# Performance work log

Hardware: AMD Instinct MI355X
Metric: run time of the kernel (lower is better)

## Reference

```python
import jax, jax.numpy as jnp
import numpy as np

B, S, D = 8, 2048, 512
MINF = 20000.0  # matches tf code's -20000.0 mask constant


def setup_inputs() -> dict:
    key = jax.random.key(0)
    k1, k2, k3 = jax.random.split(key, 3)
    x1 = jax.random.normal(k1, (B, S, D), dtype=jnp.float32)
    x2 = jax.random.normal(k2, (B, S, D), dtype=jnp.float32)
    # glorot_normal init for the learned (S, S) positional kernel
    std = np.sqrt(2.0 / (S + S)).astype(np.float32)
    kernel = jax.random.normal(k3, (S, S), dtype=jnp.float32) * std
    return {"x1": x1, "x2": x2, "kernel": kernel}


def reference(x1, x2, kernel):
    S_ = kernel.shape[0]
    # tf.matmul(kernel, inputs[i]) broadcasts (S,S) @ (B,S,D) -> (B,S,D)
    h1 = jnp.einsum('st,btd->bsd', kernel, x1)
    h2 = jnp.einsum('st,btd->bsd', kernel, x2)
    # att_scores: (B, S, S)
    scores = jnp.einsum('bsd,btd->bst', h1, h2)
    d_k = jnp.asarray(S_, dtype=scores.dtype) ** 0.5
    # upper_m[i,j] = -20000 for j > i (strictly upper), else 0; added BEFORE scaling
    row = jnp.arange(S_)
    mask = jnp.where(row[None, :] > row[:, None], -MINF, 0.0).astype(scores.dtype)
    attn = jax.nn.softmax((scores + mask) / d_k, axis=-1)
    # note: output attends over h1 (not h2), as in the original code
    return jnp.einsum('bst,btd->bsd', attn, h1)
```

## Files before the change

kernel.cpp:

```cpp
#include <hip/hip_runtime.h>
#include <hip/hip_bf16.h>

#define S_DIM 2048
#define D_DIM 512
#define B_DIM 8
#define SCALE 0.02209708691207961f

typedef __hip_bfloat16 bf16;
typedef short bf16x8 __attribute__((ext_vector_type(8)));
typedef float f32x4 __attribute__((ext_vector_type(4)));

__device__ __forceinline__ unsigned short f2b(float f) {
  __hip_bfloat16 h = __float2bfloat16(f);
  return __builtin_bit_cast(unsigned short, h);
}
__device__ __forceinline__ float b2f(unsigned short s) {
  return __bfloat162float(__builtin_bit_cast(__hip_bfloat16, s));
}

__device__ __forceinline__ void load_lds16(const void* g, void* l) {
  __builtin_amdgcn_global_load_lds((const __attribute__((address_space(1))) void*)g,
                                   (__attribute__((address_space(3))) void*)l, 16, 0, 0);
}

__global__ void convert_k(const float* __restrict__ in, bf16* __restrict__ out, int n8) {
  int i = blockIdx.x * blockDim.x + threadIdx.x;
  if (i >= n8) return;
  const float4* p = (const float4*)in;
  float4 a = p[2 * i], b = p[2 * i + 1];
  bf16x8 r;
  r[0] = f2b(a.x); r[1] = f2b(a.y); r[2] = f2b(a.z); r[3] = f2b(a.w);
  r[4] = f2b(b.x); r[5] = f2b(b.y); r[6] = f2b(b.z); r[7] = f2b(b.w);
  ((bf16x8*)out)[i] = r;
}

__global__ void transpose_f2b(const float* __restrict__ in, bf16* __restrict__ out) {
  __shared__ float tile[32][33];
  int b = blockIdx.z;
  int c0 = blockIdx.x * 32;
  int r0 = blockIdx.y * 32;
  const float* ib = in + (size_t)b * S_DIM * D_DIM;
  bf16* ob = out + (size_t)b * S_DIM * D_DIM;
  int lr = threadIdx.x >> 5, lc = threadIdx.x & 31;
#pragma unroll
  for (int i = 0; i < 4; i++)
    tile[lr + i * 8][lc] = ib[(size_t)(r0 + lr + i * 8) * D_DIM + c0 + lc];
  __syncthreads();
#pragma unroll
  for (int i = 0; i < 4; i++) {
    int cc = lr + i * 8;
    ob[(size_t)(c0 + cc) * S_DIM + r0 + lc] = __float2bfloat16(tile[lc][cc]);
  }
}

__global__ void transpose_b2b(const bf16* __restrict__ in, bf16* __restrict__ out) {
  __shared__ bf16 tile[32][33];
  int b = blockIdx.z;
  int c0 = blockIdx.x * 32;
  int r0 = blockIdx.y * 32;
  const bf16* ib = in + (size_t)b * S_DIM * D_DIM;
  bf16* ob = out + (size_t)b * S_DIM * D_DIM;
  int lr = threadIdx.x >> 5, lc = threadIdx.x & 31;
#pragma unroll
  for (int i = 0; i < 4; i++)
    tile[lr + i * 8][lc] = ib[(size_t)(r0 + lr + i * 8) * D_DIM + c0 + lc];
  __syncthreads();
#pragma unroll
  for (int i = 0; i < 4; i++) {
    int cc = lr + i * 8;
    ob[(size_t)(c0 + cc) * S_DIM + r0 + lc] = tile[lc][cc];
  }
}

template <int NT, int LDE>
__device__ __forceinline__ void core256(
    const bf16* __restrict__ Asrc, const bf16* __restrict__ Bsrc,
    char* smem, f32x4 (*acc)[4]) {
  const int tid = threadIdx.x;
  const int w = tid >> 6, L = tid & 63;
  const int l15 = L & 15, lhi = L >> 4;
  const int wr = w >> 2, wn = w & 3;

  const int srow = w * 16 + (L >> 3);
  const int sslot = ((L & 7) ^ ((L >> 3) & 7)) * 8;
  const bf16* pA[2][2];
  const bf16* pB[2][2];
#pragma unroll
  for (int h = 0; h < 2; h++)
#pragma unroll
    for (int ld = 0; ld < 2; ld++) {
      pA[h][ld] = Asrc + (size_t)(h * 128 + srow + ld * 8) * LDE + sslot;
      pB[h][ld] = Bsrc + (size_t)(h * 128 + srow + ld * 8) * LDE + sslot;
    }

  auto stage = [&](int t) {
    char* dA = smem + (t & 1) * 32768 + w * 2048;
    char* dB = smem + 65536 + (t & 1) * 32768 + w * 2048;
    const int ko = t * 64;
#pragma unroll
    for (int h = 0; h < 2; h++)
#pragma unroll
      for (int ld = 0; ld < 2; ld++) {
        load_lds16(pA[h][ld] + ko, dA + h * 16384 + ld * 1024);
        load_lds16(pB[h][ld] + ko, dB + h * 16384 + ld * 1024);
      }
  };

  const int xsw = l15 & 7;
  const int cK0 = (lhi ^ xsw) << 4;
  const int cK1 = ((4 + lhi) ^ xsw) << 4;

  stage(0);
#pragma unroll 2
  for (int t = 0; t < NT; ++t) {
    __syncthreads();
    if (t + 1 < NT) stage(t + 1);
    const char* bA = smem + (t & 1) * 32768;
    const char* bB = smem + 65536 + (t & 1) * 32768;
#pragma unroll
    for (int kk = 0; kk < 2; kk++) {
      const int cK = kk ? cK1 : cK0;
      bf16x8 af[8], bfv[4];
#pragma unroll
      for (int m = 0; m < 8; m++)
        af[m] = *(const bf16x8*)(bA + (wr * 128 + m * 16 + l15) * 128 + cK);
#pragma unroll
      for (int n = 0; n < 4; n++)
        bfv[n] = *(const bf16x8*)(bB + (wn * 64 + n * 16 + l15) * 128 + cK);
      __builtin_amdgcn_s_setprio(1);
#pragma unroll
      for (int m = 0; m < 8; m++)
#pragma unroll
        for (int n = 0; n < 4; n++)
          acc[m][n] = __builtin_amdgcn_mfma_f32_16x16x32_bf16(bfv[n], af[m], acc[m][n], 0, 0, 0);
      __builtin_amdgcn_s_setprio(0);
    }
  }
}

__global__ __launch_bounds__(512, 2) void gemm_h(
    const bf16* __restrict__ A, const bf16* __restrict__ X, bf16* __restrict__ H) {
  extern __shared__ char smem[];
  const int pid = blockIdx.x;
  const int mt = pid & 7;
  const int r_ = pid >> 3;
  const int ntile = r_ & 1;
  const int item = r_ >> 1;
  const int m0 = mt * 256, n0 = ntile * 256;
  const bf16* Asrc = A + (size_t)m0 * S_DIM;
  const bf16* Bsrc = X + (size_t)item * (D_DIM * S_DIM) + (size_t)n0 * S_DIM;
  bf16* Hi = H + (size_t)item * (S_DIM * D_DIM);

  f32x4 acc[8][4];
#pragma unroll
  for (int m = 0; m < 8; m++)
#pragma unroll
    for (int n = 0; n < 4; n++) acc[m][n] = (f32x4){0, 0, 0, 0};

  core256<32, S_DIM>(Asrc, Bsrc, smem, acc);

  const int tid = threadIdx.x;
  const int w = tid >> 6, L = tid & 63;
  const int l15 = L & 15, lhi = L >> 4;
  const int wr = w >> 2, wn = w & 3;
#pragma unroll
  for (int m = 0; m < 8; m++) {
    int grow = m0 + wr * 128 + m * 16 + l15;
#pragma unroll
    for (int n = 0; n < 4; n++) {
      int gcol = n0 + wn * 64 + n * 16 + lhi * 4;
      uint2 u;
      u.x = ((unsigned)f2b(acc[m][n][1]) << 16) | f2b(acc[m][n][0]);
      u.y = ((unsigned)f2b(acc[m][n][3]) << 16) | f2b(acc[m][n][2]);
      *(uint2*)(Hi + (size_t)grow * D_DIM + gcol) = u;
    }
  }
}

__global__ __launch_bounds__(512, 2) void gemm_score(
    const bf16* __restrict__ H1, const bf16* __restrict__ H2,
    bf16* __restrict__ E, float* __restrict__ rowsum) {
  extern __shared__ char smem[];
  const int pid = blockIdx.x;
  const int b = pid & 7;
  const int tri = pid >> 3;
  int mt = (int)((sqrtf(8.0f * (float)tri + 1.0f) - 1.0f) * 0.5f);
  while ((mt + 1) * (mt + 2) / 2 <= tri) mt++;
  while (mt * (mt + 1) / 2 > tri) mt--;
  const int nt = tri - mt * (mt + 1) / 2;
  const int m0 = mt * 256, n0 = nt * 256;
  const bool diag = (mt == nt);
  const bf16* Ab = H1 + (size_t)b * S_DIM * D_DIM;
  const bf16* Bb = H2 + (size_t)b * S_DIM * D_DIM;
  bf16* Eb = E + (size_t)b * S_DIM * S_DIM;
  float* rs = rowsum + b * S_DIM;

  f32x4 acc[8][4];
#pragma unroll
  for (int m = 0; m < 8; m++)
#pragma unroll
    for (int n = 0; n < 4; n++) acc[m][n] = (f32x4){0, 0, 0, 0};

  core256<8, D_DIM>(Ab + (size_t)m0 * D_DIM, Bb + (size_t)n0 * D_DIM, smem, acc);

  const int tid = threadIdx.x;
  const int w = tid >> 6, L = tid & 63;
  const int l15 = L & 15, lhi = L >> 4;
  const int wr = w >> 2, wn = w & 3;
#pragma unroll
  for (int m = 0; m < 8; m++) {
    int sg = m0 + wr * 128 + m * 16 + l15;
    float rp = 0.0f;
#pragma unroll
    for (int n = 0; n < 4; n++) {
      int tg0 = n0 + wn * 64 + n * 16 + lhi * 4;
      unsigned short e[4];
#pragma unroll
      for (int r = 0; r < 4; r++) {
        float v = (!diag || (tg0 + r) <= sg) ? __expf(acc[m][n][r] * SCALE) : 0.0f;
        e[r] = f2b(v);
        rp += b2f(e[r]);
      }
      uint2 u;
      u.x = ((unsigned)e[1] << 16) | e[0];
      u.y = ((unsigned)e[3] << 16) | e[2];
      *(uint2*)(Eb + (size_t)sg * S_DIM + tg0) = u;
    }
    rp += __shfl_xor(rp, 16);
    rp += __shfl_xor(rp, 32);
    if (lhi == 0) atomicAdd(rs + sg, rp);
  }
}

__global__ __launch_bounds__(256, 2) void gemm_pv(
    const bf16* __restrict__ E, const bf16* __restrict__ H1T,
    const float* __restrict__ rowsum, float* __restrict__ out) {
  extern __shared__ char smem[];
  const int pid = blockIdx.x;
  const int b = pid & 7;
  const int r_ = pid >> 3;
  const int nt = r_ & 3;
  const int mb = r_ >> 2;
  const int mt = (mb < 8) ? 2 * mb : 31 - 2 * mb;
  const int m0 = mt * 128, n0 = nt * 128;
  const int NT = (mt + 1) * 2;
  const bf16* Ab = E + (size_t)b * S_DIM * S_DIM + (size_t)m0 * S_DIM;
  const bf16* Bb = H1T + (size_t)b * D_DIM * S_DIM + (size_t)n0 * S_DIM;
  const float* rs = rowsum + b * S_DIM;
  float* Cb = out + (size_t)b * S_DIM * D_DIM;

  const int tid = threadIdx.x;
  const int w = tid >> 6, L = tid & 63;
  const int l15 = L & 15, lhi = L >> 4;
  const int wr = w >> 1, wc = w & 1;

  const int srow = w * 8 + (L >> 3);
  const int sslot = ((L & 7) ^ ((L >> 3) & 7)) * 8;
  const bf16* pA[4];
  const bf16* pB[4];
#pragma unroll
  for (int ld = 0; ld < 4; ld++) {
    pA[ld] = Ab + (size_t)(ld * 32 + srow) * S_DIM + sslot;
    pB[ld] = Bb + (size_t)(ld * 32 + srow) * S_DIM + sslot;
  }

  auto stage = [&](int t) {
    char* dA = smem + (t & 1) * 16384 + w * 1024;
    char* dB = smem + 32768 + (t & 1) * 16384 + w * 1024;
    const int ko = t * 64;
#pragma unroll
    for (int ld = 0; ld < 4; ld++) {
      load_lds16(pA[ld] + ko, dA + ld * 4096);
      load_lds16(pB[ld] + ko, dB + ld * 4096);
    }
  };

  const int xsw = l15 & 7;
  const int cK0 = (lhi ^ xsw) << 4;
  const int cK1 = ((4 + lhi) ^ xsw) << 4;

  f32x4 acc[4][4];
#pragma unroll
  for (int m = 0; m < 4; m++)
#pragma unroll
    for (int n = 0; n < 4; n++) acc[m][n] = (f32x4){0, 0, 0, 0};

  stage(0);
  for (int t = 0; t < NT; ++t) {
    __syncthreads();
    if (t + 1 < NT) stage(t + 1);
    const char* bA = smem + (t & 1) * 16384;
    const char* bB = smem + 32768 + (t & 1) * 16384;
#pragma unroll
    for (int kk = 0; kk < 2; kk++) {
      const int cK = kk ? cK1 : cK0;
      bf16x8 af[4], bfv[4];
#pragma unroll
      for (int m = 0; m < 4; m++)
        af[m] = *(const bf16x8*)(bA + (wr * 64 + m * 16 + l15) * 128 + cK);
#pragma unroll
      for (int n = 0; n < 4; n++)
        bfv[n] = *(const bf16x8*)(bB + (wc * 64 + n * 16 + l15) * 128 + cK);
      __builtin_amdgcn_s_setprio(1);
#pragma unroll
      for (int m = 0; m < 4; m++)
#pragma unroll
        for (int n = 0; n < 4; n++)
          acc[m][n] = __builtin_amdgcn_mfma_f32_16x16x32_bf16(bfv[n], af[m], acc[m][n], 0, 0, 0);
      __builtin_amdgcn_s_setprio(0);
    }
  }

#pragma unroll
  for (int m = 0; m < 4; m++) {
    int sg = m0 + wr * 64 + m * 16 + l15;
    float inv = 1.0f / rs[sg];
#pragma unroll
    for (int n = 0; n < 4; n++) {
      int gcol = n0 + wc * 64 + n * 16 + lhi * 4;
      float4 o;
      o.x = acc[m][n][0] * inv;
      o.y = acc[m][n][1] * inv;
      o.z = acc[m][n][2] * inv;
      o.w = acc[m][n][3] * inv;
      *(float4*)(Cb + (size_t)sg * D_DIM + gcol) = o;
    }
  }
}

extern "C" void kernel_launch(void* const* d_in, const int* in_sizes, int n_in,
                              void* d_out, int out_size, void* d_ws, size_t ws_size,
                              hipStream_t stream) {
  const float* x1 = (const float*)d_in[0];
  const float* x2 = (const float*)d_in[1];
  const float* km = (const float*)d_in[2];
  float* out = (float*)d_out;
  char* ws = (char*)d_ws;
  bf16* E    = (bf16*)(ws);
  bf16* Kbf  = (bf16*)(ws);
  bf16* x1t  = (bf16*)(ws + (8ull << 20));
  bf16* x2t  = (bf16*)(ws + (24ull << 20));
  bf16* h1n  = (bf16*)(ws + (64ull << 20));
  bf16* h2n  = (bf16*)(ws + (80ull << 20));
  bf16* h1t  = (bf16*)(ws + (96ull << 20));
  float* rowsum = (float*)(ws + (112ull << 20));

  convert_k<<<2048, 256, 0, stream>>>(km, Kbf, (S_DIM * S_DIM) / 8);
  transpose_f2b<<<dim3(16, 64, 8), 256, 0, stream>>>(x1, x1t);
  transpose_f2b<<<dim3(16, 64, 8), 256, 0, stream>>>(x2, x2t);
  gemm_h<<<256, 512, 131072, stream>>>(Kbf, x1t, h1n);
  transpose_b2b<<<dim3(16, 64, 8), 256, 0, stream>>>(h1n, h1t);
  hipMemsetAsync(rowsum, 0, B_DIM * S_DIM * sizeof(float), stream);
  gemm_score<<<288, 512, 131072, stream>>>(h1n, h2n, E, rowsum);
  gemm_pv<<<512, 256, 65536, stream>>>(E, h1t, rowsum, out);
}
```

Before: 200.4 us.

## Restructure gemm_h into quadrant-phased pipeline with split staging and explicit waitcnt

```diff
diff --git a/kernel.cpp b/kernel.cpp
--- a/kernel.cpp
+++ b/kernel.cpp
@@ -72,73 +72,7 @@
   }
 }
 
-template <int NT, int LDE>
-__device__ __forceinline__ void core256(
-    const bf16* __restrict__ Asrc, const bf16* __restrict__ Bsrc,
-    char* smem, f32x4 (*acc)[4]) {
-  const int tid = threadIdx.x;
-  const int w = tid >> 6, L = tid & 63;
-  const int l15 = L & 15, lhi = L >> 4;
-  const int wr = w >> 2, wn = w & 3;
-
-  const int srow = w * 16 + (L >> 3);
-  const int sslot = ((L & 7) ^ ((L >> 3) & 7)) * 8;
-  const bf16* pA[2][2];
-  const bf16* pB[2][2];
-#pragma unroll
-  for (int h = 0; h < 2; h++)
-#pragma unroll
-    for (int ld = 0; ld < 2; ld++) {
-      pA[h][ld] = Asrc + (size_t)(h * 128 + srow + ld * 8) * LDE + sslot;
-      pB[h][ld] = Bsrc + (size_t)(h * 128 + srow + ld * 8) * LDE + sslot;
-    }
-
-  auto stage = [&](int t) {
-    char* dA = smem + (t & 1) * 32768 + w * 2048;
-    char* dB = smem + 65536 + (t & 1) * 32768 + w * 2048;
-    const int ko = t * 64;
-#pragma unroll
-    for (int h = 0; h < 2; h++)
-#pragma unroll
-      for (int ld = 0; ld < 2; ld++) {
-        load_lds16(pA[h][ld] + ko, dA + h * 16384 + ld * 1024);
-        load_lds16(pB[h][ld] + ko, dB + h * 16384 + ld * 1024);
-      }
-  };
-
-  const int xsw = l15 & 7;
-  const int cK0 = (lhi ^ xsw) << 4;
-  const int cK1 = ((4 + lhi) ^ xsw) << 4;
-
-  stage(0);
-#pragma unroll 2
-  for (int t = 0; t < NT; ++t) {
-    __syncthreads();
-    if (t + 1 < NT) stage(t + 1);
-    const char* bA = smem + (t & 1) * 32768;
-    const char* bB = smem + 65536 + (t & 1) * 32768;
-#pragma unroll
-    for (int kk = 0; kk < 2; kk++) {
-      const int cK = kk ? cK1 : cK0;
-      bf16x8 af[8], bfv[4];
-#pragma unroll
-      for (int m = 0; m < 8; m++)
-        af[m] = *(const bf16x8*)(bA + (wr * 128 + m * 16 + l15) * 128 + cK);
-#pragma unroll
-      for (int n = 0; n < 4; n++)
-        bfv[n] = *(const bf16x8*)(bB + (wn * 64 + n * 16 + l15) * 128 + cK);
-      __builtin_amdgcn_s_setprio(1);
-#pragma unroll
-      for (int m = 0; m < 8; m++)
-#pragma unroll
-        for (int n = 0; n < 4; n++)
-          acc[m][n] = __builtin_amdgcn_mfma_f32_16x16x32_bf16(bfv[n], af[m], acc[m][n], 0, 0, 0);
-      __builtin_amdgcn_s_setprio(0);
-    }
-  }
-}
-
-__global__ __launch_bounds__(512, 2) void gemm_h(
+__global__ __launch_bounds__(512, 1) void gemm_h(
     const bf16* __restrict__ A, const bf16* __restrict__ X, bf16* __restrict__ H) {
   extern __shared__ char smem[];
   const int pid = blockIdx.x;
@@ -151,18 +85,115 @@
   const bf16* Bsrc = X + (size_t)item * (D_DIM * S_DIM) + (size_t)n0 * S_DIM;
   bf16* Hi = H + (size_t)item * (S_DIM * D_DIM);
 
-  f32x4 acc[8][4];
-#pragma unroll
-  for (int m = 0; m < 8; m++)
-#pragma unroll
-    for (int n = 0; n < 4; n++) acc[m][n] = (f32x4){0, 0, 0, 0};
-
-  core256<32, S_DIM>(Asrc, Bsrc, smem, acc);
-
   const int tid = threadIdx.x;
   const int w = tid >> 6, L = tid & 63;
   const int l15 = L & 15, lhi = L >> 4;
   const int wr = w >> 2, wn = w & 3;
+
+  const int srow = w * 16 + (L >> 3);
+  const int sslot = ((L & 7) ^ ((L >> 3) & 7)) * 8;
+  const bf16* pA[2][2];
+  const bf16* pB[2][2];
+#pragma unroll
+  for (int h = 0; h < 2; h++)
+#pragma unroll
+    for (int ld = 0; ld < 2; ld++) {
+      pA[h][ld] = Asrc + (size_t)(h * 128 + srow + ld * 8) * S_DIM + sslot;
+      pB[h][ld] = Bsrc + (size_t)(h * 128 + srow + ld * 8) * S_DIM + sslot;
+    }
+
+  auto stageA = [&](int t2, int half) {
+    char* d = smem + (((t2 & 1) * 2 + half) << 14) + w * 2048;
+    const int ko = t2 * 64;
+#pragma unroll
+    for (int ld = 0; ld < 2; ld++) load_lds16(pA[half][ld] + ko, d + ld * 1024);
+  };
+  auto stageB = [&](int t2, int half) {
+    char* d = smem + 65536 + (((t2 & 1) * 2 + half) << 14) + w * 2048;
+    const int ko = t2 * 64;
+#pragma unroll
+    for (int ld = 0; ld < 2; ld++) load_lds16(pB[half][ld] + ko, d + ld * 1024);
+  };
+
+  const int xsw = l15 & 7;
+  const int cK0 = (lhi ^ xsw) << 4;
+  const int cK1 = ((4 + lhi) ^ xsw) << 4;
+  const int rowA = l15 * 128;
+  const int rowB = ((wn & 1) * 64 + l15) * 128;
+
+  bf16x8 af0[4][2], af1[4][2], bfr[2][2];
+  auto readA = [&](int buf, int mh, bf16x8 (&af)[4][2]) {
+    const char* base = smem + ((buf * 2 + wr) << 14) + mh * 8192 + rowA;
+#pragma unroll
+    for (int m = 0; m < 4; m++) {
+      af[m][0] = *(const bf16x8*)(base + m * 2048 + cK0);
+      af[m][1] = *(const bf16x8*)(base + m * 2048 + cK1);
+    }
+  };
+  auto readB = [&](int buf, int nh) {
+    const char* base = smem + 65536 + ((buf * 2 + (wn >> 1)) << 14) + nh * 4096 + rowB;
+#pragma unroll
+    for (int n = 0; n < 2; n++) {
+      bfr[n][0] = *(const bf16x8*)(base + n * 2048 + cK0);
+      bfr[n][1] = *(const bf16x8*)(base + n * 2048 + cK1);
+    }
+  };
+
+  f32x4 acc[8][4];
+#pragma unroll
+  for (int m = 0; m < 8; m++)
+#pragma unroll
+    for (int n = 0; n < 4; n++) acc[m][n] = (f32x4){0, 0, 0, 0};
+
+  auto mfmaQ = [&](int mh, int nh, bf16x8 (&af)[4][2]) {
+    __builtin_amdgcn_s_setprio(1);
+#pragma unroll
+    for (int kk = 0; kk < 2; kk++)
+#pragma unroll
+      for (int m = 0; m < 4; m++)
+#pragma unroll
+        for (int n = 0; n < 2; n++)
+          acc[mh * 4 + m][nh * 2 + n] = __builtin_amdgcn_mfma_f32_16x16x32_bf16(
+              bfr[n][kk], af[m][kk], acc[mh * 4 + m][nh * 2 + n], 0, 0, 0);
+    __builtin_amdgcn_s_setprio(0);
+  };
+  auto bar = [&] {
+    asm volatile("" ::: "memory");
+    __builtin_amdgcn_s_barrier();
+    asm volatile("" ::: "memory");
+  };
+
+  const int NT = 32;
+  stageA(0, 0); stageA(0, 1); stageB(0, 0); stageB(0, 1);
+  stageA(1, 0); stageA(1, 1);
+  asm volatile("s_waitcnt vmcnt(4)" ::: "memory");
+  bar();
+
+  auto ktile = [&](int t, int buf) {
+    const bool s1 = (t + 1 < NT);
+    const bool s2 = (t + 2 < NT);
+    readA(buf, 0, af0); readB(buf, 0);
+    if (s1) stageB(t + 1, 0);
+    bar(); mfmaQ(0, 0, af0); bar();
+    readA(buf, 1, af1);
+    if (s1) stageB(t + 1, 1);
+    bar(); mfmaQ(1, 0, af1); bar();
+    readB(buf, 1);
+    if (s2) stageA(t + 2, 0);
+    bar(); mfmaQ(1, 1, af1); bar();
+    if (s2) stageA(t + 2, 1);
+    bar(); mfmaQ(0, 1, af0);
+    if (s2) asm volatile("s_waitcnt vmcnt(4)" ::: "memory");
+    else    asm volatile("s_waitcnt vmcnt(0)" ::: "memory");
+    bar();
+  };
+
+#pragma unroll 1
+  for (int t = 0; t < NT; t += 2) {
+    ktile(t, 0);
+    ktile(t + 1, 1);
+  }
+
 #pragma unroll
   for (int m = 0; m < 8; m++) {
     int grow = m0 + wr * 128 + m * 16 + l15;
@@ -173,6 +204,72 @@
       u.x = ((unsigned)f2b(acc[m][n][1]) << 16) | f2b(acc[m][n][0]);
       u.y = ((unsigned)f2b(acc[m][n][3]) << 16) | f2b(acc[m][n][2]);
       *(uint2*)(Hi + (size_t)grow * D_DIM + gcol) = u;
+    }
+  }
+}
+
+template <int NT, int LDE>
+__device__ __forceinline__ void core256(
+    const bf16* __restrict__ Asrc, const bf16* __restrict__ Bsrc,
+    char* smem, f32x4 (*acc)[4]) {
+  const int tid = threadIdx.x;
+  const int w = tid >> 6, L = tid & 63;
+  const int l15 = L & 15, lhi = L >> 4;
+  const int wr = w >> 2, wn = w & 3;
+
+  const int srow = w * 16 + (L >> 3);
+  const int sslot = ((L & 7) ^ ((L >> 3) & 7)) * 8;
+  const bf16* pA[2][2];
+  const bf16* pB[2][2];
+#pragma unroll
+  for (int h = 0; h < 2; h++)
+#pragma unroll
+    for (int ld = 0; ld < 2; ld++) {
+      pA[h][ld] = Asrc + (size_t)(h * 128 + srow + ld * 8) * LDE + sslot;
+      pB[h][ld] = Bsrc + (size_t)(h * 128 + srow + ld * 8) * LDE + sslot;
+    }
+
+  auto stage = [&](int t) {
+    char* dA = smem + (t & 1) * 32768 + w * 2048;
+    char* dB = smem + 65536 + (t & 1) * 32768 + w * 2048;
+    const int ko = t * 64;
+#pragma unroll
+    for (int h = 0; h < 2; h++)
+#pragma unroll
+      for (int ld = 0; ld < 2; ld++) {
+        load_lds16(pA[h][ld] + ko, dA + h * 16384 + ld * 1024);
+        load_lds16(pB[h][ld] + ko, dB + h * 16384 + ld * 1024);
+      }
+  };
+
+  const int xsw = l15 & 7;
+  const int cK0 = (lhi ^ xsw) << 4;
+  const int cK1 = ((4 + lhi) ^ xsw) << 4;
+
+  stage(0);
+#pragma unroll 2
+  for (int t = 0; t < NT; ++t) {
+    __syncthreads();
+    if (t + 1 < NT) stage(t + 1);
+    const char* bA = smem + (t & 1) * 32768;
+    const char* bB = smem + 65536 + (t & 1) * 32768;
+#pragma unroll
+    for (int kk = 0; kk < 2; kk++) {
+      const int cK = kk ? cK1 : cK0;
+      bf16x8 af[8], bfv[4];
+#pragma unroll
+      for (int m = 0; m < 8; m++)
+        af[m] = *(const bf16x8*)(bA + (wr * 128 + m * 16 + l15) * 128 + cK);
+#pragma unroll
+      for (int n = 0; n < 4; n++)
+        bfv[n] = *(const bf16x8*)(bB + (wn * 64 + n * 16 + l15) * 128 + cK);
+      __builtin_amdgcn_s_setprio(1);
+#pragma unroll
+      for (int m = 0; m < 8; m++)
+#pragma unroll
+        for (int n = 0; n < 4; n++)
+          acc[m][n] = __builtin_amdgcn_mfma_f32_16x16x32_bf16(bfv[n], af[m], acc[m][n], 0, 0, 0);
+      __builtin_amdgcn_s_setprio(0);
     }
   }
 }
```

After: 238.7 us. +19.2%, slower.
